# Optimization experiments

Hardware: AMD Instinct MI355X
Metric: run time of the kernel (lower is better)

## Reference

```python
import jax, jax.numpy as jnp
import numpy as np

N = 100000      # nodes
E = 1600000     # edges (avg degree 16)
F_IN = 14       # Mutagenicity num_node_features
H = 64          # hidden_channels
C = 2           # Mutagenicity num_classes
G = 512         # graphs in batch


def setup_inputs() -> dict:
    key = jax.random.key(0)
    ks = jax.random.split(key, 16)
    x = jax.random.normal(ks[0], (N, F_IN), jnp.float32)
    edge_index = jax.random.randint(ks[1], (2, E), 0, N, dtype=jnp.int32)
    batch = jnp.sort(jax.random.randint(ks[2], (N,), 0, G, dtype=jnp.int32))
    def lin(k, fi, fo):
        bound = 1.0 / np.sqrt(fi)
        kw, kb = jax.random.split(k)
        W = jax.random.uniform(kw, (fi, fo), jnp.float32, -bound, bound)
        b = jax.random.uniform(kb, (fo,), jnp.float32, -bound, bound)
        return W, b
    W1, b1 = lin(ks[3], F_IN, H)
    W2, b2 = lin(ks[4], H, H)
    W3, b3 = lin(ks[5], H, H)
    W4, b4 = lin(ks[6], H, H)
    W5, b5 = lin(ks[7], H, H)
    Wlin, blin = lin(ks[8], H, C)
    return {"x": x, "W1": W1, "b1": b1, "W2": W2, "b2": b2, "W3": W3, "b3": b3,
            "W4": W4, "b4": b4, "W5": W5, "b5": b5, "Wlin": Wlin, "blin": blin,
            "edge_index": edge_index, "batch": batch}


def _gcn_conv(h, W, b, src, dst, norm, dinv):
    # PyG GCNConv: out = D^{-1/2}(A+I)D^{-1/2} (h W) + b
    m = h @ W                                              # [N, Fout]
    agg = jax.ops.segment_sum(m[src] * norm[:, None], dst, num_segments=N)
    agg = agg + m * dinv[:, None]                          # self-loop term (norm = 1/deg)
    return agg + b


def reference(x, W1, b1, W2, b2, W3, b3, W4, b4, W5, b5, Wlin, blin, edge_index, batch):
    src, dst = edge_index[0], edge_index[1]
    # degree with self-loops (counted on target nodes, source_to_target flow)
    deg = jax.ops.segment_sum(jnp.ones(E, jnp.float32), dst, num_segments=N) + 1.0
    dinv_sqrt = jax.lax.rsqrt(deg)
    norm = dinv_sqrt[src] * dinv_sqrt[dst]                 # per-edge weight
    dinv = dinv_sqrt * dinv_sqrt                           # self-loop weight 1/deg

    h = jax.nn.relu(_gcn_conv(x, W1, b1, src, dst, norm, dinv))
    h = jax.nn.relu(_gcn_conv(h, W2, b2, src, dst, norm, dinv))
    h = jax.nn.relu(_gcn_conv(h, W3, b3, src, dst, norm, dinv))
    h = jax.nn.relu(_gcn_conv(h, W4, b4, src, dst, norm, dinv))
    h = jax.nn.relu(_gcn_conv(h, W5, b5, src, dst, norm, dinv))

    pooled = jax.ops.segment_max(h, batch, num_segments=G)  # [G, H]
    return pooled @ Wlin + blin                             # [G, C]
```

## Files before the change

### kernel.cpp

```cpp
#include <hip/hip_runtime.h>
#include <hip/hip_bf16.h>


#define HDIM 64
#define SCAN_CHUNK 1024
#define FILL_S 8


__global__ __launch_bounds__(256) void count_edges(const int* __restrict__ dst,
                                                   int* __restrict__ deg, int E) {
    int e = blockIdx.x * blockDim.x + threadIdx.x;
    if (e < E) atomicAdd(&deg[dst[e]], 1);
}

__global__ __launch_bounds__(256) void partial_sums(const int* __restrict__ deg,
                                                    int* __restrict__ psum, int n) {
    __shared__ int red[256];
    int base = blockIdx.x * SCAN_CHUNK;
    int s = 0;
    #pragma unroll
    for (int j = 0; j < 4; ++j) {
        int i = base + j * 256 + threadIdx.x;
        if (i < n) s += deg[i];
    }
    red[threadIdx.x] = s;
    __syncthreads();
    for (int off = 128; off > 0; off >>= 1) {
        if (threadIdx.x < off) red[threadIdx.x] += red[threadIdx.x + off];
        __syncthreads();
    }
    if (threadIdx.x == 0) psum[blockIdx.x] = red[0];
}

__global__ __launch_bounds__(128) void scan_partials(int* __restrict__ psum, int nb) {
    __shared__ int tmp[128];
    int t = threadIdx.x;
    int v = (t < nb) ? psum[t] : 0;
    tmp[t] = v;
    __syncthreads();
    for (int off = 1; off < 128; off <<= 1) {
        int u = (t >= off) ? tmp[t - off] : 0;
        __syncthreads();
        tmp[t] += u;
        __syncthreads();
    }
    if (t < nb) psum[t] = tmp[t] - v;
}

__global__ __launch_bounds__(256) void scan_final(const int* __restrict__ deg,
                                                  const int* __restrict__ psum,
                                                  int* __restrict__ rowptr, int n) {
    __shared__ int ts[256];
    int t = threadIdx.x;
    int base = blockIdx.x * SCAN_CHUNK + t * 4;
    int v[4];
    int s = 0;
    #pragma unroll
    for (int j = 0; j < 4; ++j) {
        int i = base + j;
        v[j] = (i < n) ? deg[i] : 0;
        s += v[j];
    }
    ts[t] = s;
    __syncthreads();
    int mine = s;
    for (int off = 1; off < 256; off <<= 1) {
        int u = (t >= off) ? ts[t - off] : 0;
        __syncthreads();
        ts[t] += u;
        __syncthreads();
    }
    int ex = ts[t] - mine + psum[blockIdx.x];
    #pragma unroll
    for (int j = 0; j < 4; ++j) {
        int i = base + j;
        if (i < n) rowptr[i] = ex;
        ex += v[j];
    }
}

__global__ __launch_bounds__(256) void node_arrays(const int* __restrict__ deg,
                                                   const int* __restrict__ rowptr,
                                                   float* __restrict__ ds,
                                                   int* __restrict__ cursor, int n) {
    int i = blockIdx.x * blockDim.x + threadIdx.x;
    if (i < n) {
        float d = (float)(deg[i] + 1);
        ds[i] = 1.0f / sqrtf(d);
        cursor[i] = rowptr[i];
    }
}

__global__ __launch_bounds__(256) void fill_csr_sharded(const int* __restrict__ src,
                                                        const int* __restrict__ dst,
                                                        int* __restrict__ cursor,
                                                        int* __restrict__ csr_src,
                                                        int E, int shard_w, int nchunks) {
    int shard = blockIdx.x & (FILL_S - 1);
    int chunk = blockIdx.x >> 3;
    int epc = (E + nchunks - 1) / nchunks;
    int e0 = chunk * epc;
    int e1 = min(e0 + epc, E);
    int lo = shard * shard_w, hi = lo + shard_w;
    for (int e = e0 + (int)threadIdx.x; e < e1; e += 256) {
        int d = dst[e];
        if (d >= lo && d < hi) {
            int pos = atomicAdd(&cursor[d], 1);
            csr_src[pos] = src[e];
        }
    }
}

__global__ __launch_bounds__(256) void pad_scale_x(const float* __restrict__ x,
                                                   const float* __restrict__ ds,
                                                   float* __restrict__ xp, int n_nodes) {
    int idx = blockIdx.x * blockDim.x + threadIdx.x;
    if (idx >= n_nodes * 16) return;
    int n = idx >> 4, j = idx & 15;
    xp[idx] = (j < 14) ? x[n * 14 + j] * ds[n] : 0.0f;
}


__global__ __launch_bounds__(256) void gather16(const float* __restrict__ xp,
                                               const int* __restrict__ rowptr,
                                               const int* __restrict__ cnt,
                                               const int* __restrict__ csr_src,
                                               const float* __restrict__ ds,
                                               float* __restrict__ agg16, int n_nodes) {
    int lane = threadIdx.x & 63;
    int sub = lane >> 4, l = lane & 15;
    int wave = blockIdx.x * (blockDim.x >> 6) + (threadIdx.x >> 6);
    int node = wave * 4 + sub;
    if (node >= n_nodes) return;
    float dsn = ds[node];
    float a0 = xp[node * 16 + l];
    float a1 = 0.f, a2 = 0.f, a3 = 0.f;
    int s = rowptr[node];
    int e = s + cnt[node];
    int i = s;
    for (; i + 3 < e; i += 4) {
        int s0 = csr_src[i], s1 = csr_src[i + 1], s2 = csr_src[i + 2], s3 = csr_src[i + 3];
        a0 += xp[s0 * 16 + l];
        a1 += xp[s1 * 16 + l];
        a2 += xp[s2 * 16 + l];
        a3 += xp[s3 * 16 + l];
    }
    for (; i < e; ++i) a0 += xp[csr_src[i] * 16 + l];
    agg16[node * 16 + l] = ((a0 + a1) + (a2 + a3)) * dsn;
}


template <int K, int KW, bool BIAS_RELU, bool SCALE>
__global__ __launch_bounds__(256) void matmul_k(const float* __restrict__ h,
                                                const float* __restrict__ W,
                                                const float* __restrict__ bias,
                                                const float* __restrict__ ds,
                                                float* __restrict__ m, int n_nodes) {
    int lane = threadIdx.x & 63;
    int wave = blockIdx.x * (blockDim.x >> 6) + (threadIdx.x >> 6);
    int n0 = wave * 4;
    if (n0 >= n_nodes) return;
    float wcol[K];
    #pragma unroll
    for (int k = 0; k < K; ++k) wcol[k] = (k < KW) ? W[k * HDIM + lane] : 0.f;
    float bl = BIAS_RELU ? bias[lane] : 0.f;

    if (n0 + 3 < n_nodes) {
        const float4* r0 = reinterpret_cast<const float4*>(h + (size_t)(n0 + 0) * K);
        const float4* r1 = reinterpret_cast<const float4*>(h + (size_t)(n0 + 1) * K);
        const float4* r2 = reinterpret_cast<const float4*>(h + (size_t)(n0 + 2) * K);
        const float4* r3 = reinterpret_cast<const float4*>(h + (size_t)(n0 + 3) * K);
        float a0[4] = {0, 0, 0, 0}, a1[4] = {0, 0, 0, 0};
        float a2[4] = {0, 0, 0, 0}, a3[4] = {0, 0, 0, 0};
        #pragma unroll
        for (int k4 = 0; k4 < K / 4; ++k4) {
            int c = k4 & 3;
            float4 v0 = r0[k4], v1 = r1[k4], v2 = r2[k4], v3 = r3[k4];
            float w0 = wcol[4 * k4 + 0], w1 = wcol[4 * k4 + 1];
            float w2 = wcol[4 * k4 + 2], w3 = wcol[4 * k4 + 3];
            a0[c] += v0.x * w0 + v0.y * w1 + v0.z * w2 + v0.w * w3;
            a1[c] += v1.x * w0 + v1.y * w1 + v1.z * w2 + v1.w * w3;
            a2[c] += v2.x * w0 + v2.y * w1 + v2.z * w2 + v2.w * w3;
            a3[c] += v3.x * w0 + v3.y * w1 + v3.z * w2 + v3.w * w3;
        }
        float s0 = (a0[0] + a0[1]) + (a0[2] + a0[3]);
        float s1 = (a1[0] + a1[1]) + (a1[2] + a1[3]);
        float s2 = (a2[0] + a2[1]) + (a2[2] + a2[3]);
        float s3 = (a3[0] + a3[1]) + (a3[2] + a3[3]);
        if constexpr (BIAS_RELU) {
            s0 = fmaxf(s0 + bl, 0.f);
            s1 = fmaxf(s1 + bl, 0.f);
            s2 = fmaxf(s2 + bl, 0.f);
            s3 = fmaxf(s3 + bl, 0.f);
        }
        if constexpr (SCALE) {
            s0 *= ds[n0 + 0];
            s1 *= ds[n0 + 1];
            s2 *= ds[n0 + 2];
            s3 *= ds[n0 + 3];
        }
        m[(size_t)(n0 + 0) * HDIM + lane] = s0;
        m[(size_t)(n0 + 1) * HDIM + lane] = s1;
        m[(size_t)(n0 + 2) * HDIM + lane] = s2;
        m[(size_t)(n0 + 3) * HDIM + lane] = s3;
    } else {
        for (int n = n0; n < n_nodes; ++n) {
            const float4* hrow = reinterpret_cast<const float4*>(h + (size_t)n * K);
            float acc[4] = {0, 0, 0, 0};
            #pragma unroll
            for (int k4 = 0; k4 < K / 4; ++k4) {
                float4 hv = hrow[k4];
                acc[k4 & 3] += hv.x * wcol[4 * k4 + 0] + hv.y * wcol[4 * k4 + 1] +
                               hv.z * wcol[4 * k4 + 2] + hv.w * wcol[4 * k4 + 3];
            }
            float s = (acc[0] + acc[1]) + (acc[2] + acc[3]);
            if constexpr (BIAS_RELU) s = fmaxf(s + bl, 0.f);
            if constexpr (SCALE) s *= ds[n];
            m[(size_t)n * HDIM + lane] = s;
        }
    }
}


__global__ __launch_bounds__(256) void gcn_gather(const float* __restrict__ m,
                                                  const int* __restrict__ rowptr,
                                                  const int* __restrict__ cnt,
                                                  const int* __restrict__ csr_src,
                                                  const float* __restrict__ ds,
                                                  const float* __restrict__ bias,
                                                  float* __restrict__ hout, int n_nodes) {
    int lane = threadIdx.x & 63;
    int node = blockIdx.x * (blockDim.x >> 6) + (threadIdx.x >> 6);
    if (node >= n_nodes) return;
    float dsn = ds[node];
    float a0 = m[node * HDIM + lane];
    float a1 = 0.f, a2 = 0.f, a3 = 0.f;
    float a4 = 0.f, a5 = 0.f, a6 = 0.f, a7 = 0.f;
    int s = rowptr[node];
    int e = s + cnt[node];
    int i = s;
    for (; i + 15 < e; i += 16) {
        int t0 = csr_src[i],      t1 = csr_src[i + 1],  t2 = csr_src[i + 2],  t3 = csr_src[i + 3];
        int t4 = csr_src[i + 4],  t5 = csr_src[i + 5],  t6 = csr_src[i + 6],  t7 = csr_src[i + 7];
        int t8 = csr_src[i + 8],  t9 = csr_src[i + 9],  ta = csr_src[i + 10], tb = csr_src[i + 11];
        int tc = csr_src[i + 12], td = csr_src[i + 13], te = csr_src[i + 14], tf = csr_src[i + 15];
        a0 += m[t0 * HDIM + lane];
        a1 += m[t1 * HDIM + lane];
        a2 += m[t2 * HDIM + lane];
        a3 += m[t3 * HDIM + lane];
        a4 += m[t4 * HDIM + lane];
        a5 += m[t5 * HDIM + lane];
        a6 += m[t6 * HDIM + lane];
        a7 += m[t7 * HDIM + lane];
        a0 += m[t8 * HDIM + lane];
        a1 += m[t9 * HDIM + lane];
        a2 += m[ta * HDIM + lane];
        a3 += m[tb * HDIM + lane];
        a4 += m[tc * HDIM + lane];
        a5 += m[td * HDIM + lane];
        a6 += m[te * HDIM + lane];
        a7 += m[tf * HDIM + lane];
    }
    for (; i + 7 < e; i += 8) {
        int t0 = csr_src[i],     t1 = csr_src[i + 1], t2 = csr_src[i + 2], t3 = csr_src[i + 3];
        int t4 = csr_src[i + 4], t5 = csr_src[i + 5], t6 = csr_src[i + 6], t7 = csr_src[i + 7];
        a0 += m[t0 * HDIM + lane];
        a1 += m[t1 * HDIM + lane];
        a2 += m[t2 * HDIM + lane];
        a3 += m[t3 * HDIM + lane];
        a4 += m[t4 * HDIM + lane];
        a5 += m[t5 * HDIM + lane];
        a6 += m[t6 * HDIM + lane];
        a7 += m[t7 * HDIM + lane];
    }
    for (; i + 1 < e; i += 2) {
        int t0 = csr_src[i], t1 = csr_src[i + 1];
        a0 += m[t0 * HDIM + lane];
        a1 += m[t1 * HDIM + lane];
    }
    if (i < e) a0 += m[csr_src[i] * HDIM + lane];
    float v = ((a0 + a1) + (a2 + a3) + ((a4 + a5) + (a6 + a7))) * dsn + bias[lane];
    hout[node * HDIM + lane] = fmaxf(v, 0.f);
}


__global__ __launch_bounds__(256) void pool_linear(const float* __restrict__ h,
                                                   const int* __restrict__ batch,
                                                   const float* __restrict__ Wlin,
                                                   const float* __restrict__ blin,
                                                   float* __restrict__ out,
                                                   int n_nodes, int n_graphs) {
    int lane = threadIdx.x & 63;
    int g = blockIdx.x * (blockDim.x >> 6) + (threadIdx.x >> 6);
    if (g >= n_graphs) return;
    int lo = 0, hi = n_nodes;
    while (lo < hi) { int mid = (lo + hi) >> 1; if (batch[mid] < g) lo = mid + 1; else hi = mid; }
    int start = lo;
    hi = n_nodes;
    while (lo < hi) { int mid = (lo + hi) >> 1; if (batch[mid] < g + 1) lo = mid + 1; else hi = mid; }
    int end = lo;
    float vmax = 0.f;
    for (int n = start; n < end; ++n) vmax = fmaxf(vmax, h[n * HDIM + lane]);
    float p0 = vmax * Wlin[lane * 2 + 0];
    float p1 = vmax * Wlin[lane * 2 + 1];
    #pragma unroll
    for (int off = 32; off > 0; off >>= 1) {
        p0 += __shfl_xor(p0, off);
        p1 += __shfl_xor(p1, off);
    }
    if (lane == 0) {
        out[g * 2 + 0] = p0 + blin[0];
        out[g * 2 + 1] = p1 + blin[1];
    }
}


extern "C" void kernel_launch(void* const* d_in, const int* in_sizes, int n_in,
                              void* d_out, int out_size, void* d_ws, size_t ws_size,
                              hipStream_t stream) {
    const float* x    = (const float*)d_in[0];
    const float* W1   = (const float*)d_in[1];
    const float* b1   = (const float*)d_in[2];
    const float* W2   = (const float*)d_in[3];
    const float* b2   = (const float*)d_in[4];
    const float* W3   = (const float*)d_in[5];
    const float* b3   = (const float*)d_in[6];
    const float* W4   = (const float*)d_in[7];
    const float* b4   = (const float*)d_in[8];
    const float* W5   = (const float*)d_in[9];
    const float* b5   = (const float*)d_in[10];
    const float* Wlin = (const float*)d_in[11];
    const float* blin = (const float*)d_in[12];
    const int* edge_index = (const int*)d_in[13];
    const int* batch      = (const int*)d_in[14];

    const int N = in_sizes[0] / 14;
    const int E = in_sizes[13] / 2;
    const int G = out_size / 2;
    const int* srcp = edge_index;
    const int* dstp = edge_index + E;

    char* ws = (char*)d_ws;
    size_t off = 0;
    auto alloc = [&](size_t bytes) -> void* {
        void* p = ws + off;
        off = (off + bytes + 255) & ~(size_t)255;
        return p;
    };
    int*   deg     = (int*)alloc((size_t)N * 4);
    int*   rowptr  = (int*)alloc((size_t)N * 4);
    int*   cursor  = (int*)alloc((size_t)N * 4);
    int*   psum    = (int*)alloc(128 * 4);
    float* ds      = (float*)alloc((size_t)N * 4);
    int*   csr_src = (int*)alloc((size_t)E * 4);
    float* buf_m   = (float*)alloc((size_t)N * HDIM * 4);
    float* buf_h   = (float*)alloc((size_t)N * HDIM * 4);
    (void)ws_size;
    float* xp    = buf_h;
    float* agg16 = buf_m;

    const int NB = (N + SCAN_CHUNK - 1) / SCAN_CHUNK;

    hipMemsetAsync(deg, 0, (size_t)N * 4, stream);
    count_edges<<<(E + 255) / 256, 256, 0, stream>>>(dstp, deg, E);
    partial_sums<<<NB, 256, 0, stream>>>(deg, psum, N);
    scan_partials<<<1, 128, 0, stream>>>(psum, NB);
    scan_final<<<NB, 256, 0, stream>>>(deg, psum, rowptr, N);
    node_arrays<<<(N + 255) / 256, 256, 0, stream>>>(deg, rowptr, ds, cursor, N);
    pad_scale_x<<<(N * 16 + 255) / 256, 256, 0, stream>>>(x, ds, xp, N);

    const int fill_chunks = 512;
    const int shard_w = (N + FILL_S - 1) / FILL_S;
    fill_csr_sharded<<<fill_chunks * FILL_S, 256, 0, stream>>>(srcp, dstp, cursor, csr_src,
                                                               E, shard_w, fill_chunks);

    const int gemm_blocks = (N + 15) / 16;
    const int gather_blocks = (N + 3) / 4;
    const int g16_blocks = (N + 15) / 16;

    gather16<<<g16_blocks, 256, 0, stream>>>(xp, rowptr, deg, csr_src, ds, agg16, N);
    matmul_k<16, 14, true, false><<<gemm_blocks, 256, 0, stream>>>(agg16, W1, b1, ds, buf_h, N);

    matmul_k<64, 64, false, true><<<gemm_blocks, 256, 0, stream>>>(buf_h, W2, b2, ds, buf_m, N);
    gcn_gather<<<gather_blocks, 256, 0, stream>>>(buf_m, rowptr, deg, csr_src, ds, b2, buf_h, N);
    matmul_k<64, 64, false, true><<<gemm_blocks, 256, 0, stream>>>(buf_h, W3, b3, ds, buf_m, N);
    gcn_gather<<<gather_blocks, 256, 0, stream>>>(buf_m, rowptr, deg, csr_src, ds, b3, buf_h, N);
    matmul_k<64, 64, false, true><<<gemm_blocks, 256, 0, stream>>>(buf_h, W4, b4, ds, buf_m, N);
    gcn_gather<<<gather_blocks, 256, 0, stream>>>(buf_m, rowptr, deg, csr_src, ds, b4, buf_h, N);
    matmul_k<64, 64, false, true><<<gemm_blocks, 256, 0, stream>>>(buf_h, W5, b5, ds, buf_m, N);
    gcn_gather<<<gather_blocks, 256, 0, stream>>>(buf_m, rowptr, deg, csr_src, ds, b5, buf_h, N);

    pool_linear<<<(G + 3) / 4, 256, 0, stream>>>(buf_h, batch, Wlin, blin, (float*)d_out, N, G);
}
```

Baseline: 819.8 us.

## Shard degree counting by destination range and stage matmul rows in LDS

The degree-count kernel is replaced by a sharded version in which each block scans a chunk of edges but only does atomics for destinations in its node shard. This mirrors the existing CSR fill and is meant to keep atomics localized per cache region. The matmul kernel now loads each wave's four input rows into shared memory with one coalesced float4 load per lane, then reads the broadcast operands from LDS instead of global memory. In exchange, each dst array is read eight times, and the matmul gains LDS traffic without a barrier, which is fine because each wave uses only its own slice.

```diff
diff --git a/kernel.cpp b/kernel.cpp
--- a/kernel.cpp
+++ b/kernel.cpp
@@ -7,10 +7,19 @@
 #define FILL_S 8
 
 
-__global__ __launch_bounds__(256) void count_edges(const int* __restrict__ dst,
-                                                   int* __restrict__ deg, int E) {
-    int e = blockIdx.x * blockDim.x + threadIdx.x;
-    if (e < E) atomicAdd(&deg[dst[e]], 1);
+__global__ __launch_bounds__(256) void count_sharded(const int* __restrict__ dst,
+                                                     int* __restrict__ deg,
+                                                     int E, int shard_w, int nchunks) {
+    int shard = blockIdx.x & (FILL_S - 1);
+    int chunk = blockIdx.x >> 3;
+    int epc = (E + nchunks - 1) / nchunks;
+    int e0 = chunk * epc;
+    int e1 = min(e0 + epc, E);
+    int lo = shard * shard_w, hi = lo + shard_w;
+    for (int e = e0 + (int)threadIdx.x; e < e1; e += 256) {
+        int d = dst[e];
+        if (d >= lo && d < hi) atomicAdd(&deg[d], 1);
+    }
 }
 
 __global__ __launch_bounds__(256) void partial_sums(const int* __restrict__ deg,
@@ -156,8 +165,10 @@
                                                 const float* __restrict__ bias,
                                                 const float* __restrict__ ds,
                                                 float* __restrict__ m, int n_nodes) {
+    __shared__ float ldsbuf[4 * 4 * K];
     int lane = threadIdx.x & 63;
-    int wave = blockIdx.x * (blockDim.x >> 6) + (threadIdx.x >> 6);
+    int wv = threadIdx.x >> 6;
+    int wave = blockIdx.x * 4 + wv;
     int n0 = wave * 4;
     if (n0 >= n_nodes) return;
     float wcol[K];
@@ -166,10 +177,17 @@
     float bl = BIAS_RELU ? bias[lane] : 0.f;
 
     if (n0 + 3 < n_nodes) {
-        const float4* r0 = reinterpret_cast<const float4*>(h + (size_t)(n0 + 0) * K);
-        const float4* r1 = reinterpret_cast<const float4*>(h + (size_t)(n0 + 1) * K);
-        const float4* r2 = reinterpret_cast<const float4*>(h + (size_t)(n0 + 2) * K);
-        const float4* r3 = reinterpret_cast<const float4*>(h + (size_t)(n0 + 3) * K);
+        float* myl = &ldsbuf[wv * 4 * K];
+        const float4* src4 = reinterpret_cast<const float4*>(h + (size_t)n0 * K);
+        if constexpr (K == 64) {
+            reinterpret_cast<float4*>(myl)[lane] = src4[lane];
+        } else {
+            if (lane < K) reinterpret_cast<float4*>(myl)[lane] = src4[lane];
+        }
+        const float4* r0 = reinterpret_cast<const float4*>(myl + 0 * K);
+        const float4* r1 = reinterpret_cast<const float4*>(myl + 1 * K);
+        const float4* r2 = reinterpret_cast<const float4*>(myl + 2 * K);
+        const float4* r3 = reinterpret_cast<const float4*>(myl + 3 * K);
         float a0[4] = {0, 0, 0, 0}, a1[4] = {0, 0, 0, 0};
         float a2[4] = {0, 0, 0, 0}, a3[4] = {0, 0, 0, 0};
         #pragma unroll
@@ -300,7 +318,7 @@
     while (lo < hi) { int mid = (lo + hi) >> 1; if (batch[mid] < g + 1) lo = mid + 1; else hi = mid; }
     int end = lo;
     float vmax = 0.f;
-    for (int n = start; n < end; ++n) vmax = fmaxf(vmax, h[n * HDIM + lane]);
+    for (int n = start; n < end; ++n) vmax = fmaxf(vmax, h[(size_t)n * HDIM + lane]);
     float p0 = vmax * Wlin[lane * 2 + 0];
     float p1 = vmax * Wlin[lane * 2 + 1];
     #pragma unroll
@@ -360,17 +378,16 @@
     float* agg16 = buf_m;
 
     const int NB = (N + SCAN_CHUNK - 1) / SCAN_CHUNK;
+    const int fill_chunks = 512;
+    const int shard_w = (N + FILL_S - 1) / FILL_S;
 
     hipMemsetAsync(deg, 0, (size_t)N * 4, stream);
-    count_edges<<<(E + 255) / 256, 256, 0, stream>>>(dstp, deg, E);
+    count_sharded<<<fill_chunks * FILL_S, 256, 0, stream>>>(dstp, deg, E, shard_w, fill_chunks);
     partial_sums<<<NB, 256, 0, stream>>>(deg, psum, N);
     scan_partials<<<1, 128, 0, stream>>>(psum, NB);
     scan_final<<<NB, 256, 0, stream>>>(deg, psum, rowptr, N);
     node_arrays<<<(N + 255) / 256, 256, 0, stream>>>(deg, rowptr, ds, cursor, N);
     pad_scale_x<<<(N * 16 + 255) / 256, 256, 0, stream>>>(x, ds, xp, N);
-
-    const int fill_chunks = 512;
-    const int shard_w = (N + FILL_S - 1) / FILL_S;
     fill_csr_sharded<<<fill_chunks * FILL_S, 256, 0, stream>>>(srcp, dstp, cursor, csr_src,
                                                                E, shard_w, fill_chunks);
 
```

Result: faster. 704.3 us (-14.1%).
